# Kernel tuning notes

Measured on AMD Instinct MI355X. Metric: run time of the kernel, lower is better.

## Reference

```python
import jax, jax.numpy as jnp
import numpy as np

THRESHOLD = 0.1
N_HEAD = 16
NEG_INF = -1e9


def setup_inputs() -> dict:
    key = jax.random.key(0)
    ks = jax.random.split(key, 8)
    B, T, C = 2, 2048, 1024
    H, D, R = N_HEAD, C // N_HEAD, 8
    return {
        "x": jax.random.normal(ks[0], (B, T, C), dtype=jnp.float32),
        "W_attn": jax.random.normal(ks[1], (C, 3 * C), dtype=jnp.float32) * 0.02,
        "W_proj": jax.random.normal(ks[2], (C, C), dtype=jnp.float32) * 0.02,
        "W_recip": jax.random.normal(ks[3], (D, R), dtype=jnp.float32) * 0.02,
        "w_std": jax.random.uniform(ks[4], (H,), dtype=jnp.float32),
        "w_rec": jax.random.uniform(ks[5], (H,), dtype=jnp.float32),
        "w_disc": jax.random.uniform(ks[6], (H,), dtype=jnp.float32),
        "d_bias": jax.random.normal(ks[7], (H, T), dtype=jnp.float32) * 0.02,
    }


def reference(x, W_attn, W_proj, W_recip, w_std, w_rec, w_disc, d_bias):
    B, T, C = x.shape
    H = N_HEAD
    D = C // H
    R = W_recip.shape[1]
    D_std = D - R

    # QKV projection (Linear without bias)
    qkv = x @ W_attn  # [B,T,3C]
    q, k, v = jnp.split(qkv, 3, axis=2)

    def to_heads(t):
        return t.reshape(B, T, H, D).transpose(0, 2, 1, 3)  # [B,H,T,D]

    q, k, v = to_heads(q), to_heads(k), to_heads(v)

    # low-rank reciprocal projections
    QW = q @ W_recip  # [B,H,T,R]
    KW = k @ W_recip

    ws = jnp.sqrt(jnp.clip(w_std, 1e-8))[:, None, None]  # [H,1,1]
    wr = jnp.sqrt(jnp.clip(w_rec, 1e-8))[:, None, None]
    use_ra = (w_rec > THRESHOLD)[:, None, None]  # [H,1,1]

    # RA heads: augmented Q/K = [ws*Q_std | wr*KW] / [ws*K_std | wr*QW]
    q_aug = jnp.concatenate([ws * q[..., :D_std], wr * KW], axis=-1)
    k_aug = jnp.concatenate([ws * k[..., :D_std], wr * QW], axis=-1)
    q_eff = jnp.where(use_ra, q_aug, ws * q)
    k_eff = jnp.where(use_ra, k_aug, ws * k)

    # mean-centered discoverability column bias: [1,H,1,T]
    d = d_bias[:, :T]
    d = d - d.mean(axis=-1, keepdims=True)
    bias = (d * w_disc[:, None])[None, :, None, :]

    scale = 1.0 / jnp.sqrt(jnp.asarray(D, dtype=x.dtype))
    scores = jnp.einsum("bhid,bhjd->bhij", q_eff, k_eff) * scale + bias
    causal = jnp.tril(jnp.ones((T, T), dtype=bool))
    scores = jnp.where(causal[None, None], scores, NEG_INF)
    attn = jax.nn.softmax(scores, axis=-1)
    out = jnp.einsum("bhij,bhjd->bhid", attn, v)  # [B,H,T,D]

    out = out.transpose(0, 2, 1, 3).reshape(B, T, C)
    return out @ W_proj
```

## Files before the change

### kernel.cpp

```cpp
#include <hip/hip_runtime.h>
#include <hip/hip_bf16.h>

#define DEVI __device__ __forceinline__

typedef __attribute__((ext_vector_type(8))) short short8;
typedef __attribute__((ext_vector_type(4))) short short4v;
typedef __attribute__((ext_vector_type(4))) float floatx4;

static constexpr int B_ = 2, T_ = 2048, C_ = 1024, H_ = 16, D_ = 64;
static constexpr float LOG2E = 1.44269504088896f;

DEVI float bf2f(unsigned short u) {
    union { unsigned int i; float f; } v; v.i = ((unsigned int)u) << 16; return v.f;
}
DEVI unsigned short f2bf(float f) {
    union { float f; unsigned int i; } v; v.f = f;
    unsigned int x = v.i;
    return (unsigned short)((x + 0x7fffu + ((x >> 16) & 1u)) >> 16);
}
DEVI unsigned int pk2bf(float lo, float hi) {
#if __has_builtin(__builtin_amdgcn_cvt_pk_bf16_f32)
    typedef __attribute__((ext_vector_type(2))) __bf16 bf16x2;
    union { bf16x2 v; unsigned int u; } r;
    r.v = __builtin_amdgcn_cvt_pk_bf16_f32(lo, hi);
    return r.u;
#else
    return (unsigned int)f2bf(lo) | ((unsigned int)f2bf(hi) << 16);
#endif
}
DEVI float fast_exp2(float x) {
#if __has_builtin(__builtin_amdgcn_exp2f)
    return __builtin_amdgcn_exp2f(x);
#else
    return __expf(x * 0.6931471805599453f);
#endif
}

DEVI void async16(const unsigned short* g, unsigned short* l) {
    __builtin_amdgcn_global_load_lds((const __attribute__((address_space(1))) void*)g,
                                     (__attribute__((address_space(3))) void*)l, 16, 0, 0);
}

DEVI void tr_body(const float* in, unsigned short* out, int K, int N, int bx, int by,
                  int tid, float (*tile)[65]) {
    int k0 = by * 64, n0 = bx * 64;
#pragma unroll
    for (int r = 0; r < 4; r++) {
        int ci = tid + r * 256;
        int row = ci >> 4, c4 = (ci & 15) * 4;
        float4 v = *(const float4*)&in[(size_t)(k0 + row) * N + n0 + c4];
        tile[row][c4 + 0] = v.x; tile[row][c4 + 1] = v.y;
        tile[row][c4 + 2] = v.z; tile[row][c4 + 3] = v.w;
    }
    __syncthreads();
#pragma unroll
    for (int r = 0; r < 2; r++) {
        int ci = tid + r * 256;
        int row = ci >> 3, c8 = (ci & 7) * 8;
        union { unsigned short u[8]; short8 s; } o;
#pragma unroll
        for (int j = 0; j < 8; j++) o.u[j] = f2bf(tile[c8 + j][row]);
        *(short8*)&out[(size_t)(n0 + row) * K + k0 + c8] = o.s;
    }
}

__global__ __launch_bounds__(256) void k_prep(const float* __restrict__ x,
                                              const float* __restrict__ W_attn,
                                              const float* __restrict__ W_proj,
                                              const float* __restrict__ d_bias,
                                              const float* __restrict__ w_disc,
                                              unsigned short* __restrict__ x_bf,
                                              unsigned short* __restrict__ wa_t,
                                              unsigned short* __restrict__ wp_t,
                                              float* __restrict__ bias) {
    __shared__ float tile[64][65];
    __shared__ float red[256];
    int bid = blockIdx.x, tid = threadIdx.x;
    if (bid < 2048) {
        int i = bid * 256 + tid;
        const float4* p = (const float4*)x + (size_t)i * 2;
        float4 a = p[0], b = p[1];
        union { unsigned short u[8]; short8 s; } r;
        r.u[0] = f2bf(a.x); r.u[1] = f2bf(a.y); r.u[2] = f2bf(a.z); r.u[3] = f2bf(a.w);
        r.u[4] = f2bf(b.x); r.u[5] = f2bf(b.y); r.u[6] = f2bf(b.z); r.u[7] = f2bf(b.w);
        *(short8*)&x_bf[(size_t)i * 8] = r.s;
    } else if (bid < 2816) {
        int idx = bid - 2048;
        tr_body(W_attn, wa_t, 1024, 3072, idx % 48, idx / 48, tid, tile);
    } else if (bid < 3072) {
        int idx = bid - 2816;
        tr_body(W_proj, wp_t, 1024, 1024, idx & 15, idx >> 4, tid, tile);
    } else {
        int h = bid - 3072;
        float s = 0.f;
        for (int t = tid; t < T_; t += 256) s += d_bias[h * T_ + t];
        red[tid] = s;
        __syncthreads();
        for (int st = 128; st > 0; st >>= 1) {
            if (tid < st) red[tid] += red[tid + st];
            __syncthreads();
        }
        float mean = red[0] * (1.0f / T_);
        float wd = w_disc[h] * LOG2E;
        for (int t = tid; t < T_; t += 256) bias[h * T_ + t] = (d_bias[h * T_ + t] - mean) * wd;
    }
}

template <typename OUT>
__global__ __launch_bounds__(256) void k_gemm(const unsigned short* __restrict__ A,
                                              const unsigned short* __restrict__ Bt,
                                              OUT* __restrict__ C, int M, int N, int K) {
    __shared__ __align__(16) unsigned short As[128 * 32];
    __shared__ __align__(16) unsigned short Bs[128 * 32];
    int m0 = blockIdx.y * 128, n0 = blockIdx.x * 128;
    int tid = threadIdx.x, l = tid & 63, w = tid >> 6;
    int wm = (w >> 1) * 64, wn = (w & 1) * 64;
    int lm = l & 15, lq = l >> 4;
    floatx4 acc[4][4];
#pragma unroll
    for (int a = 0; a < 4; a++)
#pragma unroll
        for (int b = 0; b < 4; b++) acc[a][b] = {0.f, 0.f, 0.f, 0.f};

    for (int k0 = 0; k0 < K; k0 += 32) {
        __syncthreads();
#pragma unroll
        for (int r = 0; r < 2; r++) {
            int ci = tid + r * 256;
            int row = ci >> 2, off = (ci & 3) * 8;
            async16(&A[(size_t)(m0 + row) * K + k0 + off], &As[row * 32 + off]);
            async16(&Bt[(size_t)(n0 + row) * K + k0 + off], &Bs[row * 32 + off]);
        }
        __syncthreads();
        short8 af[4], bf[4];
#pragma unroll
        for (int t = 0; t < 4; t++) af[t] = *(short8*)&As[(wm + t * 16 + lm) * 32 + lq * 8];
#pragma unroll
        for (int t = 0; t < 4; t++) bf[t] = *(short8*)&Bs[(wn + t * 16 + lm) * 32 + lq * 8];
#pragma unroll
        for (int tm = 0; tm < 4; tm++)
#pragma unroll
            for (int tn = 0; tn < 4; tn++)
                acc[tm][tn] = __builtin_amdgcn_mfma_f32_16x16x32_bf16(af[tm], bf[tn], acc[tm][tn], 0, 0, 0);
    }
#pragma unroll
    for (int tm = 0; tm < 4; tm++)
#pragma unroll
        for (int tn = 0; tn < 4; tn++) {
            int row = m0 + wm + tm * 16 + lq * 4;
            int col = n0 + wn + tn * 16 + lm;
#pragma unroll
            for (int r = 0; r < 4; r++) {
                float v = acc[tm][tn][r];
                if constexpr (sizeof(OUT) == 2) C[(size_t)(row + r) * N + col] = (OUT)f2bf(v);
                else                            C[(size_t)(row + r) * N + col] = v;
            }
        }
}

__global__ __launch_bounds__(256) void k_gemm64(const unsigned short* __restrict__ A,
                                                const unsigned short* __restrict__ Bt,
                                                float* __restrict__ C, int M, int N, int K) {
    __shared__ __align__(16) unsigned short As[128 * 32];
    __shared__ __align__(16) unsigned short Bs[64 * 32];
    int m0 = blockIdx.y * 128, n0 = blockIdx.x * 64;
    int tid = threadIdx.x, l = tid & 63, w = tid >> 6;
    int wm = w * 32;
    int lm = l & 15, lq = l >> 4;
    floatx4 acc[2][4];
#pragma unroll
    for (int a = 0; a < 2; a++)
#pragma unroll
        for (int b = 0; b < 4; b++) acc[a][b] = {0.f, 0.f, 0.f, 0.f};

    for (int k0 = 0; k0 < K; k0 += 32) {
        __syncthreads();
#pragma unroll
        for (int r = 0; r < 2; r++) {
            int ci = tid + r * 256;
            int row = ci >> 2, off = (ci & 3) * 8;
            async16(&A[(size_t)(m0 + row) * K + k0 + off], &As[row * 32 + off]);
        }
        {
            int row = tid >> 2, off = (tid & 3) * 8;
            async16(&Bt[(size_t)(n0 + row) * K + k0 + off], &Bs[row * 32 + off]);
        }
        __syncthreads();
        short8 af[2], bf[4];
#pragma unroll
        for (int t = 0; t < 2; t++) af[t] = *(short8*)&As[(wm + t * 16 + lm) * 32 + lq * 8];
#pragma unroll
        for (int t = 0; t < 4; t++) bf[t] = *(short8*)&Bs[(t * 16 + lm) * 32 + lq * 8];
#pragma unroll
        for (int tm = 0; tm < 2; tm++)
#pragma unroll
            for (int tn = 0; tn < 4; tn++)
                acc[tm][tn] = __builtin_amdgcn_mfma_f32_16x16x32_bf16(af[tm], bf[tn], acc[tm][tn], 0, 0, 0);
    }
#pragma unroll
    for (int tm = 0; tm < 2; tm++)
#pragma unroll
        for (int tn = 0; tn < 4; tn++) {
            int row = m0 + wm + tm * 16 + lq * 4;
            int col = n0 + tn * 16 + lm;
#pragma unroll
            for (int r = 0; r < 4; r++) C[(size_t)(row + r) * N + col] = acc[tm][tn][r];
        }
}

DEVI void build_body(const unsigned short* qkv, const float* Wr, const float* w_std,
                     const float* w_rec, unsigned short* qe, unsigned short* ke, int g) {
    int t = g & (T_ - 1), h = (g >> 11) & (H_ - 1), b = g >> 15;
    float ws = sqrtf(fmaxf(w_std[h], 1e-8f));
    float wr = sqrtf(fmaxf(w_rec[h], 1e-8f));
    bool ra = w_rec[h] > 0.1f;
    const unsigned short* qrow = qkv + (size_t)(b * T_ + t) * 3072 + h * 64;
    const unsigned short* krow = qrow + 1024;
    float q[64], k[64];
#pragma unroll
    for (int i = 0; i < 8; i++) {
        short8 qv = *(const short8*)&qrow[i * 8];
        short8 kv = *(const short8*)&krow[i * 8];
#pragma unroll
        for (int j = 0; j < 8; j++) {
            q[i * 8 + j] = bf2f((unsigned short)qv[j]);
            k[i * 8 + j] = bf2f((unsigned short)kv[j]);
        }
    }
    float QW[8], KW[8];
#pragma unroll
    for (int r = 0; r < 8; r++) { QW[r] = 0.f; KW[r] = 0.f; }
#pragma unroll
    for (int d = 0; d < 64; d++)
#pragma unroll
        for (int r = 0; r < 8; r++) {
            QW[r] += q[d] * Wr[d * 8 + r];
            KW[r] += k[d] * Wr[d * 8 + r];
        }
    const float qscale = 0.125f * LOG2E;
    size_t tbase = (size_t)(b * H_ + h) * 131072 + (size_t)(t >> 4) * 1024 + (size_t)(t & 15) * 8;
#pragma unroll
    for (int i = 0; i < 8; i++) {
        union { unsigned short u[8]; short8 s; } uq, uk;
#pragma unroll
        for (int j = 0; j < 8; j++) {
            int d = i * 8 + j;
            float qv, kv;
            if (ra && d >= 56) { qv = wr * KW[d - 56]; kv = wr * QW[d - 56]; }
            else               { qv = ws * q[d];       kv = ws * k[d]; }
            uq.u[j] = f2bf(qv * qscale);
            uk.u[j] = f2bf(kv);
        }
        size_t off = tbase + (size_t)(i >> 2) * 512 + (size_t)(i & 3) * 128;
        *(short8*)&qe[off] = uq.s;
        *(short8*)&ke[off] = uk.s;
    }
}

__global__ __launch_bounds__(256) void k_bv(const unsigned short* __restrict__ qkv,
                                            const float* __restrict__ W_recip,
                                            const float* __restrict__ w_std,
                                            const float* __restrict__ w_rec,
                                            unsigned short* __restrict__ qe,
                                            unsigned short* __restrict__ ke,
                                            unsigned short* __restrict__ vt) {
    __shared__ float Wr[64 * 8];
    int bid = blockIdx.x, tid = threadIdx.x;
    if (bid < 256) {
        for (int i = tid; i < 512; i += 256) Wr[i] = W_recip[i];
        __syncthreads();
        build_body(qkv, Wr, w_std, w_rec, qe, ke, bid * 256 + tid);
    } else {
        int g = bid - 256;
        int tchunk = g & 63;
        int h = (g >> 6) & 15, b = g >> 10;
        int d = tid & 63, tg = tid >> 6;
        int t0 = tchunk * 32 + tg * 8;
        union { unsigned short u[8]; short8 s; } v;
#pragma unroll
        for (int i = 0; i < 8; i++)
            v.u[i] = qkv[(size_t)(b * T_ + t0 + i) * 3072 + 2048 + h * 64 + d];
        size_t off = (size_t)((b * H_ + h)) * 131072 + (size_t)tchunk * 2048 +
                     (size_t)(d >> 4) * 512 + (size_t)tg * 128 + (size_t)(d & 15) * 8;
        *(short8*)&vt[off] = v.s;
    }
}

DEVI void exp_pack(float sv[4][4], float& l_part, unsigned int pk[4][2]) {
#pragma unroll
    for (int js = 0; js < 4; js++)
#pragma unroll
        for (int r = 0; r < 4; r++) {
            float p = fast_exp2(sv[js][r]);
            sv[js][r] = p;
            l_part += p;
        }
#pragma unroll
    for (int js = 0; js < 4; js++) {
        pk[js][0] = pk2bf(sv[js][0], sv[js][1]);
        pk[js][1] = pk2bf(sv[js][2], sv[js][3]);
    }
}

DEVI short8 make_pf(const unsigned int pk[4][2], int c, int srcLo, int srcHi, bool hi) {
    int a0 = __shfl((int)pk[2 * c][0], srcLo);
    int a1 = __shfl((int)pk[2 * c][1], srcLo);
    int a2 = __shfl((int)pk[2 * c][0], srcHi);
    int a3 = __shfl((int)pk[2 * c][1], srcHi);
    int b0 = __shfl((int)pk[2 * c + 1][0], srcLo);
    int b1 = __shfl((int)pk[2 * c + 1][1], srcLo);
    int b2 = __shfl((int)pk[2 * c + 1][0], srcHi);
    int b3 = __shfl((int)pk[2 * c + 1][1], srcHi);
    union { int i[4]; short8 s; } pf;
    pf.i[0] = hi ? b0 : a0;
    pf.i[1] = hi ? b1 : a1;
    pf.i[2] = hi ? b2 : a2;
    pf.i[3] = hi ? b3 : a3;
    return pf.s;
}

struct KF { short8 lo[4]; short8 hi[4]; };

__global__ __launch_bounds__(256) void k_attn(const unsigned short* __restrict__ qe,
                                              const unsigned short* __restrict__ ke,
                                              const unsigned short* __restrict__ vt,
                                              const float* __restrict__ bias,
                                              unsigned short* __restrict__ obf) {
    int bh = blockIdx.y;
    int b = bh >> 4, h = bh & 15;
    int tid = threadIdx.x, l = tid & 63, w = tid >> 6;
    int lm = l & 15, lq = l >> 4;
    int l8 = l * 8;
    const size_t hb = (size_t)bh * 131072;
    const unsigned short* qeh = qe + hb;
    const unsigned short* keh = ke + hb;
    const unsigned short* vth = vt + hb;
    const float* biash = bias + h * T_;

    int gA = blockIdx.x * 4 + w;
    int gB = 127 - gA;
    int itA = (gA >> 2) + 1, itB = (gB >> 2) + 1;
    int irowA = gA * 16 + lm, irowB = gB * 16 + lm;

    short8 qA0 = *(const short8*)(qeh + (size_t)gA * 1024 + l8);
    short8 qA1 = *(const short8*)(qeh + (size_t)gA * 1024 + 512 + l8);
    short8 qB0 = *(const short8*)(qeh + (size_t)gB * 1024 + l8);
    short8 qB1 = *(const short8*)(qeh + (size_t)gB * 1024 + 512 + l8);

    floatx4 OA[4], OB[4];
#pragma unroll
    for (int i = 0; i < 4; i++) { OA[i] = {0.f, 0.f, 0.f, 0.f}; OB[i] = {0.f, 0.f, 0.f, 0.f}; }
    float lA = 0.f, lB = 0.f;

    const int srcLo = ((lq & 1) * 2) * 16 + lm;
    const int srcHi = srcLo + 16;
    const bool hi = (lq >> 1) & 1;

    KF kfa, kfb;
#pragma unroll
    for (int js = 0; js < 4; js++) {
        const unsigned short* kp = keh + (size_t)js * 1024 + l8;
        kfa.lo[js] = *(const short8*)kp;
        kfa.hi[js] = *(const short8*)(kp + 512);
    }

    auto step = [&](int s, KF& cur, KF& nxt) {
        int j0 = s * 64;
        bool doA = (s < itA);
        bool maskA = (s == itA - 1);
        bool maskB = (s == itB - 1);
        {
            const unsigned short* kb = keh + (size_t)(s + 1) * 4096 + l8;
#pragma unroll
            for (int js = 0; js < 4; js++) {
                nxt.lo[js] = *(const short8*)(kb + js * 1024);
                nxt.hi[js] = *(const short8*)(kb + js * 1024 + 512);
            }
        }
        short8 vfr[2][4];
#pragma unroll
        for (int c = 0; c < 2; c++)
#pragma unroll
            for (int dt = 0; dt < 4; dt++)
                vfr[c][dt] = *(const short8*)(vth + (size_t)((j0 >> 5) + c) * 2048 + dt * 512 + l8);
        float bv[4][4];
#pragma unroll
        for (int js = 0; js < 4; js++) {
            float4 bj = *(const float4*)&biash[j0 + js * 16 + lq * 4];
            bv[js][0] = bj.x; bv[js][1] = bj.y; bv[js][2] = bj.z; bv[js][3] = bj.w;
        }
        floatx4 sb4[4], sa4[4];
#pragma unroll
        for (int js = 0; js < 4; js++) {
            floatx4 sb = {0.f, 0.f, 0.f, 0.f};
            sb = __builtin_amdgcn_mfma_f32_16x16x32_bf16(cur.lo[js], qB0, sb, 0, 0, 0);
            sb = __builtin_amdgcn_mfma_f32_16x16x32_bf16(cur.hi[js], qB1, sb, 0, 0, 0);
            sb4[js] = sb;
        }
        if (doA) {
#pragma unroll
            for (int js = 0; js < 4; js++) {
                floatx4 sa = {0.f, 0.f, 0.f, 0.f};
                sa = __builtin_amdgcn_mfma_f32_16x16x32_bf16(cur.lo[js], qA0, sa, 0, 0, 0);
                sa = __builtin_amdgcn_mfma_f32_16x16x32_bf16(cur.hi[js], qA1, sa, 0, 0, 0);
                sa4[js] = sa;
            }
        }
        float svB[4][4];
#pragma unroll
        for (int js = 0; js < 4; js++)
#pragma unroll
            for (int r = 0; r < 4; r++) svB[js][r] = sb4[js][r] + bv[js][r];
        if (maskB) {
#pragma unroll
            for (int js = 0; js < 4; js++) {
                int jb = j0 + js * 16 + lq * 4;
#pragma unroll
                for (int r = 0; r < 4; r++)
                    if (jb + r > irowB) svB[js][r] = -1e9f;
            }
        }
        unsigned int pkB[4][2];
        exp_pack(svB, lB, pkB);

        if (doA) {
            float svA[4][4];
#pragma unroll
            for (int js = 0; js < 4; js++)
#pragma unroll
                for (int r = 0; r < 4; r++) svA[js][r] = sa4[js][r] + bv[js][r];
            if (maskA) {
#pragma unroll
                for (int js = 0; js < 4; js++) {
                    int jb = j0 + js * 16 + lq * 4;
#pragma unroll
                    for (int r = 0; r < 4; r++)
                        if (jb + r > irowA) svA[js][r] = -1e9f;
                }
            }
            unsigned int pkA[4][2];
            exp_pack(svA, lA, pkA);
#pragma unroll
            for (int c = 0; c < 2; c++) {
                short8 pfA = make_pf(pkA, c, srcLo, srcHi, hi);
                short8 pfB = make_pf(pkB, c, srcLo, srcHi, hi);
#pragma unroll
                for (int dt = 0; dt < 4; dt++) {
                    OA[dt] = __builtin_amdgcn_mfma_f32_16x16x32_bf16(vfr[c][dt], pfA, OA[dt], 0, 0, 0);
                    OB[dt] = __builtin_amdgcn_mfma_f32_16x16x32_bf16(vfr[c][dt], pfB, OB[dt], 0, 0, 0);
                }
            }
        } else {
#pragma unroll
            for (int c = 0; c < 2; c++) {
                short8 pfB = make_pf(pkB, c, srcLo, srcHi, hi);
#pragma unroll
                for (int dt = 0; dt < 4; dt++)
                    OB[dt] = __builtin_amdgcn_mfma_f32_16x16x32_bf16(vfr[c][dt], pfB, OB[dt], 0, 0, 0);
            }
        }
    };

    int s = 0;
    for (; s + 2 <= itB; s += 2) {
        step(s, kfa, kfb);
        step(s + 1, kfb, kfa);
    }
    if (s < itB) step(s, kfa, kfb);

    lA += __shfl_xor(lA, 16); lA += __shfl_xor(lA, 32);
    lB += __shfl_xor(lB, 16); lB += __shfl_xor(lB, 32);
    {
        float inv = 1.0f / lA;
        unsigned short* orow = obf + (size_t)(b * T_ + irowA) * C_ + h * 64;
#pragma unroll
        for (int dt = 0; dt < 4; dt++) {
            union { unsigned short u[4]; short4v s4; } o;
#pragma unroll
            for (int r = 0; r < 4; r++) o.u[r] = f2bf(OA[dt][r] * inv);
            *(short4v*)&orow[dt * 16 + lq * 4] = o.s4;
        }
    }
    {
        float inv = 1.0f / lB;
        unsigned short* orow = obf + (size_t)(b * T_ + irowB) * C_ + h * 64;
#pragma unroll
        for (int dt = 0; dt < 4; dt++) {
            union { unsigned short u[4]; short4v s4; } o;
#pragma unroll
            for (int r = 0; r < 4; r++) o.u[r] = f2bf(OB[dt][r] * inv);
            *(short4v*)&orow[dt * 16 + lq * 4] = o.s4;
        }
    }
}

extern "C" void kernel_launch(void* const* d_in, const int* in_sizes, int n_in,
                              void* d_out, int out_size, void* d_ws, size_t ws_size,
                              hipStream_t stream) {
    const float* x       = (const float*)d_in[0];
    const float* W_attn  = (const float*)d_in[1];
    const float* W_proj  = (const float*)d_in[2];
    const float* W_recip = (const float*)d_in[3];
    const float* w_std   = (const float*)d_in[4];
    const float* w_rec   = (const float*)d_in[5];
    const float* w_disc  = (const float*)d_in[6];
    const float* d_bias  = (const float*)d_in[7];

    char* ws = (char*)d_ws;
    size_t o = 0;
    unsigned short* x_bf = (unsigned short*)(ws + o); o += (size_t)4096 * 1024 * 2;
    unsigned short* wa_t = (unsigned short*)(ws + o); o += (size_t)3072 * 1024 * 2;
    unsigned short* wp_t = (unsigned short*)(ws + o); o += (size_t)1024 * 1024 * 2;
    unsigned short* qkv  = (unsigned short*)(ws + o); o += (size_t)4096 * 3072 * 2;
    unsigned short* qe   = (unsigned short*)(ws + o); o += (size_t)32 * 2048 * 64 * 2;
    unsigned short* ke   = (unsigned short*)(ws + o); o += (size_t)32 * 2048 * 64 * 2;
    unsigned short* vt   = (unsigned short*)(ws + o); o += (size_t)32 * 2048 * 64 * 2;
    unsigned short* obf  = (unsigned short*)(ws + o); o += (size_t)4096 * 1024 * 2;
    float* bias          = (float*)(ws + o);          o += (size_t)16 * 2048 * 4;

    k_prep<<<3088, 256, 0, stream>>>(x, W_attn, W_proj, d_bias, w_disc, x_bf, wa_t, wp_t, bias);
    k_gemm<unsigned short><<<dim3(24, 32), 256, 0, stream>>>(x_bf, wa_t, qkv, 4096, 3072, 1024);
    k_bv<<<2304, 256, 0, stream>>>(qkv, W_recip, w_std, w_rec, qe, ke, vt);
    k_attn<<<dim3(16, 32), 256, 0, stream>>>(qe, ke, vt, bias, obf);
    k_gemm64<<<dim3(16, 32), 256, 0, stream>>>(obf, wp_t, (float*)d_out, 4096, 1024, 1024);
}
```

Before: 208.7 us.

## Split attention KV loop across wave pairs and reduce partials in LDS

Each pair of waves now shares one query-row pair (A/B). The two waves process alternating 64-key blocks, so each wave walks half the KV sequence. Partial O and row-sum accumulators are combined through shared memory after a block barrier, and the attention grid doubles to 1024 blocks. This targets the long serial KV loop per wave and low occupancy on 256 CUs, at the cost of an LDS reduction, a barrier and doubled Q/bias loads. It relies on the softmax using a fixed max (no running max), so the partial sums can simply be added.

```diff
diff --git a/kernel.cpp b/kernel.cpp
--- a/kernel.cpp
+++ b/kernel.cpp
@@ -326,9 +326,12 @@
                                               const unsigned short* __restrict__ vt,
                                               const float* __restrict__ bias,
                                               unsigned short* __restrict__ obf) {
+    __shared__ __align__(16) float psum[2][64][36];
     int bh = blockIdx.y;
     int b = bh >> 4, h = bh & 15;
     int tid = threadIdx.x, l = tid & 63, w = tid >> 6;
+    int pairL = w >> 1;
+    int phase = w & 1;
     int lm = l & 15, lq = l >> 4;
     int l8 = l * 8;
     const size_t hb = (size_t)bh * 131072;
@@ -337,7 +340,7 @@
     const unsigned short* vth = vt + hb;
     const float* biash = bias + h * T_;
 
-    int gA = blockIdx.x * 4 + w;
+    int gA = blockIdx.x * 2 + pairL;
     int gB = 127 - gA;
     int itA = (gA >> 2) + 1, itB = (gB >> 2) + 1;
     int irowA = gA * 16 + lm, irowB = gB * 16 + lm;
@@ -359,7 +362,7 @@
     KF kfa, kfb;
 #pragma unroll
     for (int js = 0; js < 4; js++) {
-        const unsigned short* kp = keh + (size_t)js * 1024 + l8;
+        const unsigned short* kp = keh + (size_t)phase * 4096 + (size_t)js * 1024 + l8;
         kfa.lo[js] = *(const short8*)kp;
         kfa.hi[js] = *(const short8*)(kp + 512);
     }
@@ -370,7 +373,7 @@
         bool maskA = (s == itA - 1);
         bool maskB = (s == itB - 1);
         {
-            const unsigned short* kb = keh + (size_t)(s + 1) * 4096 + l8;
+            const unsigned short* kb = keh + (size_t)(s + 2) * 4096 + l8;
 #pragma unroll
             for (int js = 0; js < 4; js++) {
                 nxt.lo[js] = *(const short8*)(kb + js * 1024);
@@ -461,12 +464,32 @@
         }
     };
 
-    int s = 0;
-    for (; s + 2 <= itB; s += 2) {
+    int s = phase;
+    for (; s + 2 < itB; s += 4) {
         step(s, kfa, kfb);
-        step(s + 1, kfb, kfa);
+        step(s + 2, kfb, kfa);
     }
     if (s < itB) step(s, kfa, kfb);
+
+    if (phase == 1) {
+        float* dst = psum[pairL][l];
+#pragma unroll
+        for (int dt = 0; dt < 4; dt++) *(floatx4*)&dst[dt * 4] = OA[dt];
+#pragma unroll
+        for (int dt = 0; dt < 4; dt++) *(floatx4*)&dst[16 + dt * 4] = OB[dt];
+        dst[32] = lA; dst[33] = lB;
+    }
+    __syncthreads();
+    if (phase == 1) return;
+    {
+        const float* src = psum[pairL][l];
+#pragma unroll
+        for (int dt = 0; dt < 4; dt++) {
+            OA[dt] += *(const floatx4*)&src[dt * 4];
+            OB[dt] += *(const floatx4*)&src[16 + dt * 4];
+        }
+        lA += src[32]; lB += src[33];
+    }
 
     lA += __shfl_xor(lA, 16); lA += __shfl_xor(lA, 32);
     lB += __shfl_xor(lB, 16); lB += __shfl_xor(lB, 32);
@@ -521,6 +544,6 @@
     k_prep<<<3088, 256, 0, stream>>>(x, W_attn, W_proj, d_bias, w_disc, x_bf, wa_t, wp_t, bias);
     k_gemm<unsigned short><<<dim3(24, 32), 256, 0, stream>>>(x_bf, wa_t, qkv, 4096, 3072, 1024);
     k_bv<<<2304, 256, 0, stream>>>(qkv, W_recip, w_std, w_rec, qe, ke, vt);
-    k_attn<<<dim3(16, 32), 256, 0, stream>>>(qe, ke, vt, bias, obf);
+    k_attn<<<dim3(32, 32), 256, 0, stream>>>(qe, ke, vt, bias, obf);
     k_gemm64<<<dim3(16, 32), 256, 0, stream>>>(obf, wp_t, (float*)d_out, 4096, 1024, 1024);
 }
```

Measured after the change: 209.4 us. No clear change (+0.4%).

## Stage K, V and bias tiles through double-buffered LDS with async loads

Applied to the files above, without the earlier changes.

Each wave used to load the K, V and bias tiles straight from global memory into registers, so all four waves of a block fetched the same data separately. Now the block cooperatively copies each 64-key tile of K, V and bias into a double-buffered LDS area using global_load_lds. The next tile is prefetched while the current one is computed, and the waves read their fragments from LDS. This cuts redundant global/L2 traffic, at the cost of a block-wide barrier per step, extra LDS reads, and a dependence on the async LDS writes having completed before the barrier.

```diff
diff --git a/kernel.cpp b/kernel.cpp
--- a/kernel.cpp
+++ b/kernel.cpp
@@ -39,6 +39,10 @@
 DEVI void async16(const unsigned short* g, unsigned short* l) {
     __builtin_amdgcn_global_load_lds((const __attribute__((address_space(1))) void*)g,
                                      (__attribute__((address_space(3))) void*)l, 16, 0, 0);
+}
+DEVI void async4(const float* g, float* l) {
+    __builtin_amdgcn_global_load_lds((const __attribute__((address_space(1))) void*)g,
+                                     (__attribute__((address_space(3))) void*)l, 4, 0, 0);
 }
 
 DEVI void tr_body(const float* in, unsigned short* out, int K, int N, int bx, int by,
@@ -319,13 +323,14 @@
     return pf.s;
 }
 
-struct KF { short8 lo[4]; short8 hi[4]; };
-
 __global__ __launch_bounds__(256) void k_attn(const unsigned short* __restrict__ qe,
                                               const unsigned short* __restrict__ ke,
                                               const unsigned short* __restrict__ vt,
                                               const float* __restrict__ bias,
                                               unsigned short* __restrict__ obf) {
+    __shared__ __align__(16) unsigned short Ks[2][4096];
+    __shared__ __align__(16) unsigned short Vs[2][4096];
+    __shared__ __align__(16) float Bsh[2][64];
     int bh = blockIdx.y;
     int b = bh >> 4, h = bh & 15;
     int tid = threadIdx.x, l = tid & 63, w = tid >> 6;
@@ -356,53 +361,52 @@
     const int srcHi = srcLo + 16;
     const bool hi = (lq >> 1) & 1;
 
-    KF kfa, kfb;
-#pragma unroll
-    for (int js = 0; js < 4; js++) {
-        const unsigned short* kp = keh + (size_t)js * 1024 + l8;
-        kfa.lo[js] = *(const short8*)kp;
-        kfa.hi[js] = *(const short8*)(kp + 512);
-    }
-
-    auto step = [&](int s, KF& cur, KF& nxt) {
+    auto stage = [&](int s, int t) {
+        const unsigned short* kg = keh + (size_t)s * 4096;
+        const unsigned short* vg = vth + (size_t)s * 4096;
+        int s0 = (w * 2 + 0) * 512 + l8;
+        int s1 = (w * 2 + 1) * 512 + l8;
+        async16(kg + s0, &Ks[t][s0]);
+        async16(kg + s1, &Ks[t][s1]);
+        async16(vg + s0, &Vs[t][s0]);
+        async16(vg + s1, &Vs[t][s1]);
+        if (w == 0) async4(biash + s * 64 + l, &Bsh[t][l]);
+    };
+
+    auto step = [&](int s, int cur) {
+        const unsigned short* Kc = Ks[cur];
+        const unsigned short* Vc = Vs[cur];
+        const float* Bc = Bsh[cur];
         int j0 = s * 64;
         bool doA = (s < itA);
         bool maskA = (s == itA - 1);
         bool maskB = (s == itB - 1);
-        {
-            const unsigned short* kb = keh + (size_t)(s + 1) * 4096 + l8;
-#pragma unroll
-            for (int js = 0; js < 4; js++) {
-                nxt.lo[js] = *(const short8*)(kb + js * 1024);
-                nxt.hi[js] = *(const short8*)(kb + js * 1024 + 512);
-            }
-        }
-        short8 vfr[2][4];
-#pragma unroll
-        for (int c = 0; c < 2; c++)
-#pragma unroll
-            for (int dt = 0; dt < 4; dt++)
-                vfr[c][dt] = *(const short8*)(vth + (size_t)((j0 >> 5) + c) * 2048 + dt * 512 + l8);
+        short8 klo[4], khi[4];
+#pragma unroll
+        for (int js = 0; js < 4; js++) {
+            klo[js] = *(const short8*)&Kc[js * 1024 + l8];
+            khi[js] = *(const short8*)&Kc[js * 1024 + 512 + l8];
+        }
         float bv[4][4];
 #pragma unroll
         for (int js = 0; js < 4; js++) {
-            float4 bj = *(const float4*)&biash[j0 + js * 16 + lq * 4];
+            float4 bj = *(const float4*)&Bc[js * 16 + lq * 4];
             bv[js][0] = bj.x; bv[js][1] = bj.y; bv[js][2] = bj.z; bv[js][3] = bj.w;
         }
         floatx4 sb4[4], sa4[4];
 #pragma unroll
         for (int js = 0; js < 4; js++) {
             floatx4 sb = {0.f, 0.f, 0.f, 0.f};
-            sb = __builtin_amdgcn_mfma_f32_16x16x32_bf16(cur.lo[js], qB0, sb, 0, 0, 0);
-            sb = __builtin_amdgcn_mfma_f32_16x16x32_bf16(cur.hi[js], qB1, sb, 0, 0, 0);
+            sb = __builtin_amdgcn_mfma_f32_16x16x32_bf16(klo[js], qB0, sb, 0, 0, 0);
+            sb = __builtin_amdgcn_mfma_f32_16x16x32_bf16(khi[js], qB1, sb, 0, 0, 0);
             sb4[js] = sb;
         }
         if (doA) {
 #pragma unroll
             for (int js = 0; js < 4; js++) {
                 floatx4 sa = {0.f, 0.f, 0.f, 0.f};
-                sa = __builtin_amdgcn_mfma_f32_16x16x32_bf16(cur.lo[js], qA0, sa, 0, 0, 0);
-                sa = __builtin_amdgcn_mfma_f32_16x16x32_bf16(cur.hi[js], qA1, sa, 0, 0, 0);
+                sa = __builtin_amdgcn_mfma_f32_16x16x32_bf16(klo[js], qA0, sa, 0, 0, 0);
+                sa = __builtin_amdgcn_mfma_f32_16x16x32_bf16(khi[js], qA1, sa, 0, 0, 0);
                 sa4[js] = sa;
             }
         }
@@ -442,31 +446,43 @@
             exp_pack(svA, lA, pkA);
 #pragma unroll
             for (int c = 0; c < 2; c++) {
+                short8 vfr[4];
+#pragma unroll
+                for (int dt = 0; dt < 4; dt++)
+                    vfr[dt] = *(const short8*)&Vc[c * 2048 + dt * 512 + l8];
                 short8 pfA = make_pf(pkA, c, srcLo, srcHi, hi);
                 short8 pfB = make_pf(pkB, c, srcLo, srcHi, hi);
 #pragma unroll
                 for (int dt = 0; dt < 4; dt++) {
-                    OA[dt] = __builtin_amdgcn_mfma_f32_16x16x32_bf16(vfr[c][dt], pfA, OA[dt], 0, 0, 0);
-                    OB[dt] = __builtin_amdgcn_mfma_f32_16x16x32_bf16(vfr[c][dt], pfB, OB[dt], 0, 0, 0);
+                    OA[dt] = __builtin_amdgcn_mfma_f32_16x16x32_bf16(vfr[dt], pfA, OA[dt], 0, 0, 0);
+                    OB[dt] = __builtin_amdgcn_mfma_f32_16x16x32_bf16(vfr[dt], pfB, OB[dt], 0, 0, 0);
                 }
             }
         } else {
 #pragma unroll
             for (int c = 0; c < 2; c++) {
+                short8 vfr[4];
+#pragma unroll
+                for (int dt = 0; dt < 4; dt++)
+                    vfr[dt] = *(const short8*)&Vc[c * 2048 + dt * 512 + l8];
                 short8 pfB = make_pf(pkB, c, srcLo, srcHi, hi);
 #pragma unroll
                 for (int dt = 0; dt < 4; dt++)
-                    OB[dt] = __builtin_amdgcn_mfma_f32_16x16x32_bf16(vfr[c][dt], pfB, OB[dt], 0, 0, 0);
+                    OB[dt] = __builtin_amdgcn_mfma_f32_16x16x32_bf16(vfr[dt], pfB, OB[dt], 0, 0, 0);
             }
         }
     };
 
-    int s = 0;
-    for (; s + 2 <= itB; s += 2) {
-        step(s, kfa, kfb);
-        step(s + 1, kfb, kfa);
-    }
-    if (s < itB) step(s, kfa, kfb);
+    stage(0, 0);
+    __syncthreads();
+    int cur = 0;
+    for (int s = 0; s < itB; s++) {
+        int sp = (s + 1 < itB) ? s + 1 : s;
+        stage(sp, cur ^ 1);
+        step(s, cur);
+        __syncthreads();
+        cur ^= 1;
+    }
 
     lA += __shfl_xor(lA, 16); lA += __shfl_xor(lA, 32);
     lB += __shfl_xor(lB, 16); lB += __shfl_xor(lB, 32);
```

New measurement: 211.9 us. About the same (+1.5%).

## Fold head scaling and reciprocal projection into QKV weights, write attention layouts directly

Applied to the files above, without the earlier changes.

Folds the per-head std/rec scaling, the softmax scale, and the low-rank W_recip projection into the transposed QKV weight matrix during prep. The reciprocal columns become W_attn·W_recip, computed once per head. The QKV GEMM epilogue now writes q_eff, k_eff and the transposed V straight into the tiled layouts the attention kernel reads. This removes the intermediate qkv buffer and the separate k_bv kernel launch with its extra global round trip. The cost is scattered 2-byte epilogue stores and extra serial prep work for the 32 projection blocks.

```diff
diff --git a/kernel.cpp b/kernel.cpp
--- a/kernel.cpp
+++ b/kernel.cpp
@@ -42,7 +42,7 @@
 }
 
 DEVI void tr_body(const float* in, unsigned short* out, int K, int N, int bx, int by,
-                  int tid, float (*tile)[65]) {
+                  int tid, float (*tile)[65], float scale, bool skiphi) {
     int k0 = by * 64, n0 = bx * 64;
 #pragma unroll
     for (int r = 0; r < 4; r++) {
@@ -57,9 +57,10 @@
     for (int r = 0; r < 2; r++) {
         int ci = tid + r * 256;
         int row = ci >> 3, c8 = (ci & 7) * 8;
+        if (skiphi && row >= 56) continue;
         union { unsigned short u[8]; short8 s; } o;
 #pragma unroll
-        for (int j = 0; j < 8; j++) o.u[j] = f2bf(tile[c8 + j][row]);
+        for (int j = 0; j < 8; j++) o.u[j] = f2bf(tile[c8 + j][row] * scale);
         *(short8*)&out[(size_t)(n0 + row) * K + k0 + c8] = o.s;
     }
 }
@@ -69,6 +70,9 @@
                                               const float* __restrict__ W_proj,
                                               const float* __restrict__ d_bias,
                                               const float* __restrict__ w_disc,
+                                              const float* __restrict__ W_recip,
+                                              const float* __restrict__ w_std,
+                                              const float* __restrict__ w_rec,
                                               unsigned short* __restrict__ x_bf,
                                               unsigned short* __restrict__ wa_t,
                                               unsigned short* __restrict__ wp_t,
@@ -86,11 +90,15 @@
         *(short8*)&x_bf[(size_t)i * 8] = r.s;
     } else if (bid < 2816) {
         int idx = bid - 2048;
-        tr_body(W_attn, wa_t, 1024, 3072, idx % 48, idx / 48, tid, tile);
+        int bx = idx % 48, by = idx / 48;
+        int sec = bx >> 4, h = bx & 15;
+        float ws = sqrtf(fmaxf(w_std[h], 1e-8f));
+        float sc = (sec == 0) ? ws * (0.125f * LOG2E) : (sec == 1 ? ws : 1.0f);
+        tr_body(W_attn, wa_t, 1024, 3072, bx, by, tid, tile, sc, sec < 2);
     } else if (bid < 3072) {
         int idx = bid - 2816;
-        tr_body(W_proj, wp_t, 1024, 1024, idx & 15, idx >> 4, tid, tile);
-    } else {
+        tr_body(W_proj, wp_t, 1024, 1024, idx & 15, idx >> 4, tid, tile, 1.0f, false);
+    } else if (bid < 3088) {
         int h = bid - 3072;
         float s = 0.f;
         for (int t = tid; t < T_; t += 256) s += d_bias[h * T_ + t];
@@ -103,13 +111,47 @@
         float mean = red[0] * (1.0f / T_);
         float wd = w_disc[h] * LOG2E;
         for (int t = tid; t < T_; t += 256) bias[h * T_ + t] = (d_bias[h * T_ + t] - mean) * wd;
-    }
-}
-
-template <typename OUT>
-__global__ __launch_bounds__(256) void k_gemm(const unsigned short* __restrict__ A,
-                                              const unsigned short* __restrict__ Bt,
-                                              OUT* __restrict__ C, int M, int N, int K) {
+    } else {
+        int idx = bid - 3088;
+        int h = idx & 15, side = idx >> 4;
+        float* WrS = &tile[0][0];
+        for (int i = tid; i < 512; i += 256) WrS[i] = W_recip[i];
+        __syncthreads();
+        float wrv = sqrtf(fmaxf(w_rec[h], 1e-8f));
+        float wsv = sqrtf(fmaxf(w_std[h], 1e-8f));
+        bool ra = w_rec[h] > 0.1f;
+        float sc = (side == 0 ? 0.125f * LOG2E : 1.0f) * (ra ? wrv : wsv);
+        int dst0 = side * 1024 + h * 64 + 56;
+        for (int kk = tid; kk < 1024; kk += 256) {
+            const float* srow = W_attn + (size_t)kk * 3072;
+            float out[8];
+            if (ra) {
+                int sc0 = (1 - side) * 1024 + h * 64;
+#pragma unroll
+                for (int r = 0; r < 8; r++) out[r] = 0.f;
+                for (int dd = 0; dd < 64; dd++) {
+                    float v = srow[sc0 + dd];
+#pragma unroll
+                    for (int r = 0; r < 8; r++) out[r] += v * WrS[dd * 8 + r];
+                }
+            } else {
+                int sc0 = side * 1024 + h * 64 + 56;
+#pragma unroll
+                for (int r = 0; r < 8; r++) out[r] = srow[sc0 + r];
+            }
+#pragma unroll
+            for (int r = 0; r < 8; r++)
+                wa_t[(size_t)(dst0 + r) * 1024 + kk] = f2bf(sc * out[r]);
+        }
+    }
+}
+
+__global__ __launch_bounds__(256) void k_gemm_qkv(const unsigned short* __restrict__ A,
+                                                  const unsigned short* __restrict__ Bt,
+                                                  unsigned short* __restrict__ qe,
+                                                  unsigned short* __restrict__ ke,
+                                                  unsigned short* __restrict__ vt,
+                                                  int M, int N, int K) {
     __shared__ __align__(16) unsigned short As[128 * 32];
     __shared__ __align__(16) unsigned short Bs[128 * 32];
     int m0 = blockIdx.y * 128, n0 = blockIdx.x * 128;
@@ -143,19 +185,41 @@
             for (int tn = 0; tn < 4; tn++)
                 acc[tm][tn] = __builtin_amdgcn_mfma_f32_16x16x32_bf16(af[tm], bf[tn], acc[tm][tn], 0, 0, 0);
     }
-#pragma unroll
-    for (int tm = 0; tm < 4; tm++)
-#pragma unroll
-        for (int tn = 0; tn < 4; tn++) {
-            int row = m0 + wm + tm * 16 + lq * 4;
-            int col = n0 + wn + tn * 16 + lm;
-#pragma unroll
-            for (int r = 0; r < 4; r++) {
-                float v = acc[tm][tn][r];
-                if constexpr (sizeof(OUT) == 2) C[(size_t)(row + r) * N + col] = (OUT)f2bf(v);
-                else                            C[(size_t)(row + r) * N + col] = v;
-            }
-        }
+    int sec = blockIdx.x >> 3;
+    int b = blockIdx.y >> 4;
+    int hbase = (n0 & 1023) >> 6;
+    int head = hbase + (wn >> 6);
+    size_t bhbase = (size_t)(b * 16 + head) * 131072;
+    unsigned short* dst = (sec == 0) ? qe : (sec == 1) ? ke : vt;
+    if (sec < 2) {
+#pragma unroll
+        for (int tm = 0; tm < 4; tm++)
+#pragma unroll
+            for (int tn = 0; tn < 4; tn++) {
+                int d = tn * 16 + lm;
+                int tloc = (m0 & 2047) + wm + tm * 16;
+                size_t base = bhbase + (size_t)(tloc >> 4) * 1024 +
+                              (size_t)(d >> 5) * 512 + (size_t)((d >> 3) & 3) * 128 + (d & 7);
+#pragma unroll
+                for (int r = 0; r < 4; r++)
+                    dst[base + (size_t)(lq * 4 + r) * 8] = f2bf(acc[tm][tn][r]);
+            }
+    } else {
+#pragma unroll
+        for (int tm = 0; tm < 4; tm++)
+#pragma unroll
+            for (int tn = 0; tn < 4; tn++) {
+                int d = tn * 16 + lm;
+                int tloc = (m0 & 2047) + wm + tm * 16 + lq * 4;
+                size_t base = bhbase + (size_t)(tloc >> 5) * 2048 +
+                              (size_t)(d >> 4) * 512 + (size_t)((tloc >> 3) & 3) * 128 +
+                              (size_t)(d & 15) * 8 + (lq & 1) * 4;
+                union { unsigned short u[4]; short4v s4; } o;
+#pragma unroll
+                for (int r = 0; r < 4; r++) o.u[r] = f2bf(acc[tm][tn][r]);
+                *(short4v*)&dst[base] = o.s4;
+            }
+    }
 }
 
 __global__ __launch_bounds__(256) void k_gemm64(const unsigned short* __restrict__ A,
@@ -206,84 +270,6 @@
 #pragma unroll
             for (int r = 0; r < 4; r++) C[(size_t)(row + r) * N + col] = acc[tm][tn][r];
         }
-}
-
-DEVI void build_body(const unsigned short* qkv, const float* Wr, const float* w_std,
-                     const float* w_rec, unsigned short* qe, unsigned short* ke, int g) {
-    int t = g & (T_ - 1), h = (g >> 11) & (H_ - 1), b = g >> 15;
-    float ws = sqrtf(fmaxf(w_std[h], 1e-8f));
-    float wr = sqrtf(fmaxf(w_rec[h], 1e-8f));
-    bool ra = w_rec[h] > 0.1f;
-    const unsigned short* qrow = qkv + (size_t)(b * T_ + t) * 3072 + h * 64;
-    const unsigned short* krow = qrow + 1024;
-    float q[64], k[64];
-#pragma unroll
-    for (int i = 0; i < 8; i++) {
-        short8 qv = *(const short8*)&qrow[i * 8];
-        short8 kv = *(const short8*)&krow[i * 8];
-#pragma unroll
-        for (int j = 0; j < 8; j++) {
-            q[i * 8 + j] = bf2f((unsigned short)qv[j]);
-            k[i * 8 + j] = bf2f((unsigned short)kv[j]);
-        }
-    }
-    float QW[8], KW[8];
-#pragma unroll
-    for (int r = 0; r < 8; r++) { QW[r] = 0.f; KW[r] = 0.f; }
-#pragma unroll
-    for (int d = 0; d < 64; d++)
-#pragma unroll
-        for (int r = 0; r < 8; r++) {
-            QW[r] += q[d] * Wr[d * 8 + r];
-            KW[r] += k[d] * Wr[d * 8 + r];
-        }
-    const float qscale = 0.125f * LOG2E;
-    size_t tbase = (size_t)(b * H_ + h) * 131072 + (size_t)(t >> 4) * 1024 + (size_t)(t & 15) * 8;
-#pragma unroll
-    for (int i = 0; i < 8; i++) {
-        union { unsigned short u[8]; short8 s; } uq, uk;
-#pragma unroll
-        for (int j = 0; j < 8; j++) {
-            int d = i * 8 + j;
-            float qv, kv;
-            if (ra && d >= 56) { qv = wr * KW[d - 56]; kv = wr * QW[d - 56]; }
-            else               { qv = ws * q[d];       kv = ws * k[d]; }
-            uq.u[j] = f2bf(qv * qscale);
-            uk.u[j] = f2bf(kv);
-        }
-        size_t off = tbase + (size_t)(i >> 2) * 512 + (size_t)(i & 3) * 128;
-        *(short8*)&qe[off] = uq.s;
-        *(short8*)&ke[off] = uk.s;
-    }
-}
-
-__global__ __launch_bounds__(256) void k_bv(const unsigned short* __restrict__ qkv,
-                                            const float* __restrict__ W_recip,
-                                            const float* __restrict__ w_std,
-                                            const float* __restrict__ w_rec,
-                                            unsigned short* __restrict__ qe,
-                                            unsigned short* __restrict__ ke,
-                                            unsigned short* __restrict__ vt) {
-    __shared__ float Wr[64 * 8];
-    int bid = blockIdx.x, tid = threadIdx.x;
-    if (bid < 256) {
-        for (int i = tid; i < 512; i += 256) Wr[i] = W_recip[i];
-        __syncthreads();
-        build_body(qkv, Wr, w_std, w_rec, qe, ke, bid * 256 + tid);
-    } else {
-        int g = bid - 256;
-        int tchunk = g & 63;
-        int h = (g >> 6) & 15, b = g >> 10;
-        int d = tid & 63, tg = tid >> 6;
-        int t0 = tchunk * 32 + tg * 8;
-        union { unsigned short u[8]; short8 s; } v;
-#pragma unroll
-        for (int i = 0; i < 8; i++)
-            v.u[i] = qkv[(size_t)(b * T_ + t0 + i) * 3072 + 2048 + h * 64 + d];
-        size_t off = (size_t)((b * H_ + h)) * 131072 + (size_t)tchunk * 2048 +
-                     (size_t)(d >> 4) * 512 + (size_t)tg * 128 + (size_t)(d & 15) * 8;
-        *(short8*)&vt[off] = v.s;
-    }
 }
 
 DEVI void exp_pack(float sv[4][4], float& l_part, unsigned int pk[4][2]) {
@@ -511,16 +497,15 @@
     unsigned short* x_bf = (unsigned short*)(ws + o); o += (size_t)4096 * 1024 * 2;
     unsigned short* wa_t = (unsigned short*)(ws + o); o += (size_t)3072 * 1024 * 2;
     unsigned short* wp_t = (unsigned short*)(ws + o); o += (size_t)1024 * 1024 * 2;
-    unsigned short* qkv  = (unsigned short*)(ws + o); o += (size_t)4096 * 3072 * 2;
     unsigned short* qe   = (unsigned short*)(ws + o); o += (size_t)32 * 2048 * 64 * 2;
     unsigned short* ke   = (unsigned short*)(ws + o); o += (size_t)32 * 2048 * 64 * 2;
     unsigned short* vt   = (unsigned short*)(ws + o); o += (size_t)32 * 2048 * 64 * 2;
     unsigned short* obf  = (unsigned short*)(ws + o); o += (size_t)4096 * 1024 * 2;
     float* bias          = (float*)(ws + o);          o += (size_t)16 * 2048 * 4;
 
-    k_prep<<<3088, 256, 0, stream>>>(x, W_attn, W_proj, d_bias, w_disc, x_bf, wa_t, wp_t, bias);
-    k_gemm<unsigned short><<<dim3(24, 32), 256, 0, stream>>>(x_bf, wa_t, qkv, 4096, 3072, 1024);
-    k_bv<<<2304, 256, 0, stream>>>(qkv, W_recip, w_std, w_rec, qe, ke, vt);
+    k_prep<<<3120, 256, 0, stream>>>(x, W_attn, W_proj, d_bias, w_disc, W_recip, w_std, w_rec,
+                                     x_bf, wa_t, wp_t, bias);
+    k_gemm_qkv<<<dim3(24, 32), 256, 0, stream>>>(x_bf, wa_t, qe, ke, vt, 4096, 3072, 1024);
     k_attn<<<dim3(16, 32), 256, 0, stream>>>(qe, ke, vt, bias, obf);
     k_gemm64<<<dim3(16, 32), 256, 0, stream>>>(obf, wp_t, (float*)d_out, 4096, 1024, 1024);
 }
```

New measurement: 209.6 us. Within noise of the previous version (+0.5%).
